# Optimization experiments

Measured on AMD Instinct MI355X. Metric: run time of the kernel, lower is better.

## Reference

```python
import jax, jax.numpy as jnp
import numpy as np
from jax import lax

DILATIONS = (1, 3, 9, 9, 3, 1)  # six mid blocks after the 1x1 input conv


def bilinear_sample(fm, verts):
    # fm: [B,H,W,C]; verts: [B,N,2] in [-1,1]; axis 0 of verts maps to H, axis 1 to W.
    # Matches jax.scipy.ndimage.map_coordinates(order=1, mode='constant'):
    # each out-of-bounds corner contributes 0.
    B, H, W, C = fm.shape
    scale = jnp.array([H - 1, W - 1], fm.dtype) / 2.0
    coords = (verts + 1.0) * scale  # [B,N,2]
    vy, vx = coords[..., 0], coords[..., 1]
    y0 = jnp.floor(vy)
    x0 = jnp.floor(vx)
    wy = (vy - y0)[..., None]
    wx = (vx - x0)[..., None]
    y0i = y0.astype(jnp.int32)
    x0i = x0.astype(jnp.int32)
    fm_flat = fm.reshape(B, H * W, C)

    def corner(yi, xi):
        valid = (yi >= 0) & (yi < H) & (xi >= 0) & (xi < W)
        idx = jnp.clip(yi, 0, H - 1) * W + jnp.clip(xi, 0, W - 1)  # [B,N]
        vals = jnp.take_along_axis(fm_flat, idx[..., None], axis=1)  # [B,N,C]
        return jnp.where(valid[..., None], vals, jnp.zeros((), fm.dtype))

    return ((1 - wy) * (1 - wx) * corner(y0i, x0i)
            + (1 - wy) * wx * corner(y0i, x0i + 1)
            + wy * (1 - wx) * corner(y0i + 1, x0i)
            + wy * wx * corner(y0i + 1, x0i + 1))


def conv1d(x, w, b, dil):
    # x: [B,N,Cin], w: [K,Cin,Cout]; flax nnx.Conv default: stride 1, SAME padding.
    out = lax.conv_general_dilated(x, w, (1,), 'SAME', rhs_dilation=(dil,),
                                   dimension_numbers=('NWC', 'WIO', 'NWC'))
    return out if b is None else out + b


def setup_inputs() -> dict:
    key = jax.random.key(0)
    ks = jax.random.split(key, 8)
    B, N, H, W, Cf, Ch = 16, 1024, 256, 256, 126, 512
    D = Cf + 2
    vertices = jax.random.uniform(ks[0], (B, N, 2), jnp.float32, -1.0, 1.0)
    feature_map = jax.random.normal(ks[1], (B, H, W, Cf), jnp.float32)
    w0 = jax.random.normal(ks[2], (1, D, Ch), jnp.float32) / np.float32(np.sqrt(D))
    b0 = jnp.zeros((Ch,), jnp.float32)
    ws = jax.random.normal(ks[3], (6, 3, Ch, Ch), jnp.float32) / np.float32(np.sqrt(3 * Ch))
    bs = jnp.zeros((6, Ch), jnp.float32)
    w_off = jax.random.normal(ks[4], (1, Ch, 2), jnp.float32) / np.float32(np.sqrt(Ch))
    return {"vertices": vertices, "feature_map": feature_map,
            "w0": w0, "b0": b0, "ws": ws, "bs": bs, "w_off": w_off}


def reference(vertices, feature_map, w0, b0, ws, bs, w_off):
    feat = bilinear_sample(feature_map, vertices)          # [B,N,Cf]
    x = jnp.concatenate([feat, vertices], axis=-1)         # [B,N,Cf+2]
    x = jax.nn.relu(conv1d(x, w0, b0, 1))                  # 1x1 input conv
    for i, dil in enumerate(DILATIONS):                    # fixed 6-layer stack
        x = jax.nn.relu(conv1d(x, ws[i], bs[i], dil))
    return conv1d(x, w_off, None, 1)                       # [B,N,2] offsets
```

## Files before the change

### kernel.cpp

```cpp
#include <hip/hip_runtime.h>

typedef __attribute__((ext_vector_type(4))) float f32x4;
typedef __attribute__((ext_vector_type(8))) _Float16 f16x8;

#define BM 128
#define BK 64

#define OFF_W0T 0
#define OFF_WT  131072
#define OFF_X0  (OFF_WT + 6*512*1536*2)
#define OFF_Y0  (OFF_X0 + 16384*128*2)
#define OFF_Y1  (OFF_Y0 + 16*1056*512*2)

__device__ __forceinline__ void load_lds16(const void* g, void* s) {
    __builtin_amdgcn_global_load_lds(
        (const __attribute__((address_space(1))) void*)g,
        (__attribute__((address_space(3))) void*)s, 16, 0, 0);
}

__global__ __launch_bounds__(256)
void wprep(const float* __restrict__ ws, const float* __restrict__ w0,
           _Float16* __restrict__ wt, _Float16* __restrict__ w0t)
{
    __shared__ float t[64][65];
    const int tid = threadIdx.x;
    const int tr = tid >> 6;
    const int tc = tid & 63;
    const int z = blockIdx.z;
    if (z < 18) {
        const int l = z / 3, tp = z % 3;
        const float* src = ws + (size_t)z * 512 * 512;
        const int ci0 = blockIdx.y * 64, co0 = blockIdx.x * 64;
        #pragma unroll
        for (int i = 0; i < 16; ++i) { int r = i*4 + tr; t[r][tc] = src[(ci0 + r)*512 + co0 + tc]; }
        __syncthreads();
        _Float16* dst = wt + (size_t)l * 512 * 1536;
        #pragma unroll
        for (int i = 0; i < 16; ++i) { int r = i*4 + tr; dst[(co0 + r)*1536 + tp*512 + ci0 + tc] = (_Float16)t[tc][r]; }
    } else {
        if (blockIdx.y >= 2) return;
        const int ci0 = blockIdx.y * 64, co0 = blockIdx.x * 64;
        #pragma unroll
        for (int i = 0; i < 16; ++i) { int r = i*4 + tr; t[r][tc] = w0[(ci0 + r)*512 + co0 + tc]; }
        __syncthreads();
        #pragma unroll
        for (int i = 0; i < 16; ++i) { int r = i*4 + tr; w0t[(co0 + r)*128 + ci0 + tc] = (_Float16)t[tc][r]; }
    }
}

__global__ __launch_bounds__(256)
void zeropad(_Float16* __restrict__ Y0, _Float16* __restrict__ Y1)
{
    const int i = blockIdx.x * 256 + threadIdx.x;
    const unsigned c2   = i & 255;
    const unsigned t2   = ((unsigned)i) >> 8;
    const unsigned prow = t2 & 31;
    const unsigned b    = (t2 >> 5) & 15;
    const unsigned buf  = t2 >> 9;
    const unsigned row  = prow < 16 ? prow : (1024 + prow);
    unsigned* p = (unsigned*)(buf ? Y1 : Y0);
    p[((size_t)b * 1056 + row) * 256 + c2] = 0u;
}

__global__ __launch_bounds__(256)
void sample_kernel(const float* __restrict__ verts, const float* __restrict__ fm,
                   _Float16* __restrict__ X0)
{
    const int p = blockIdx.x * 4 + (threadIdx.x >> 6);
    const int lane = threadIdx.x & 63;
    const int b = p >> 10;
    const float vy = verts[p*2], vx = verts[p*2 + 1];
    const float cy = (vy + 1.f) * 127.5f;
    const float cx = (vx + 1.f) * 127.5f;
    const float fy = floorf(cy), fx = floorf(cx);
    const int y0 = (int)fy, x0 = (int)fx;
    const float wy = cy - fy, wx = cx - fx;
    float w00 = (1.f - wy) * (1.f - wx), w01 = (1.f - wy) * wx;
    float w10 = wy * (1.f - wx),         w11 = wy * wx;
    const bool vy0 = (unsigned)y0 < 256u, vy1 = (unsigned)(y0 + 1) < 256u;
    const bool vx0 = (unsigned)x0 < 256u, vx1 = (unsigned)(x0 + 1) < 256u;
    w00 = (vy0 && vx0) ? w00 : 0.f;
    w01 = (vy0 && vx1) ? w01 : 0.f;
    w10 = (vy1 && vx0) ? w10 : 0.f;
    w11 = (vy1 && vx1) ? w11 : 0.f;
    const int yc0 = min(max(y0, 0), 255), yc1 = min(max(y0 + 1, 0), 255);
    const int xc0 = min(max(x0, 0), 255), xc1 = min(max(x0 + 1, 0), 255);
    const float* base = fm + (size_t)b * (256 * 256 * 126);
    const float* p00 = base + (yc0 * 256 + xc0) * 126;
    const float* p01 = base + (yc0 * 256 + xc1) * 126;
    const float* p10 = base + (yc1 * 256 + xc0) * 126;
    const float* p11 = base + (yc1 * 256 + xc1) * 126;
    _Float16* xr = X0 + (size_t)p * 128;
    for (int c = lane; c < 126; c += 64) {
        float a = w00 * p00[c] + w01 * p01[c] + w10 * p10[c] + w11 * p11[c];
        xr[c] = (_Float16)a;
    }
    if (lane < 2) xr[126 + lane] = (_Float16)(lane ? vx : vy);
}

template<int KTOT>
__global__ __launch_bounds__(256)
void conv_gemm(const _Float16* __restrict__ A, int a_row_stride, int a_batch_stride,
               const _Float16* __restrict__ WT, const float* __restrict__ bias,
               _Float16* __restrict__ Out, int o_row_stride, int o_batch_stride,
               int dil)
{
    __shared__ _Float16 Ald[BM * BK];
    __shared__ _Float16 Bld[BM * BK];
    const int tid  = threadIdx.x;
    const int wid  = tid >> 6;
    const int lane = tid & 63;
    const int b    = blockIdx.x >> 3;
    const int n0   = (blockIdx.x & 7) * BM;
    const int co0  = blockIdx.y * BM;
    const int wm   = wid >> 1, wn = wid & 1;

    const _Float16* Ab = A + (size_t)b * a_batch_stride + (size_t)n0 * a_row_stride;

    f32x4 acc[4][4] = {};

    const int srow = lane >> 3;
    const int scol = (lane & 7) * 8;

    for (int ks = 0; ks < KTOT / BK; ++ks) {
        int ci0, shift;
        if (KTOT == 128) { ci0 = ks * 64; shift = 0; }
        else             { int t = ks >> 3; ci0 = (ks & 7) * 64; shift = (t - 1) * dil; }
        const _Float16* Arow = Ab + (long)shift * a_row_stride + ci0 + scol;
        const _Float16* Brow = WT + (size_t)co0 * KTOT + ks * 64 + scol;
        #pragma unroll
        for (int i = 0; i < 4; ++i) {
            const int r0 = wid * 32 + i * 8;
            load_lds16(Arow + (size_t)(r0 + srow) * a_row_stride, &Ald[r0 * BK]);
            load_lds16(Brow + (size_t)(r0 + srow) * KTOT,         &Bld[r0 * BK]);
        }
        __syncthreads();
        #pragma unroll
        for (int kf = 0; kf < 2; ++kf) {
            f16x8 af[4], bfr[4];
            #pragma unroll
            for (int f = 0; f < 4; ++f) {
                af[f]  = *(const f16x8*)&Ald[(wm*64 + f*16 + (lane & 15)) * BK + kf*32 + (lane >> 4) * 8];
                bfr[f] = *(const f16x8*)&Bld[(wn*64 + f*16 + (lane & 15)) * BK + kf*32 + (lane >> 4) * 8];
            }
            #pragma unroll
            for (int m = 0; m < 4; ++m)
                #pragma unroll
                for (int n = 0; n < 4; ++n)
                    acc[m][n] = __builtin_amdgcn_mfma_f32_16x16x32_f16(af[m], bfr[n], acc[m][n], 0, 0, 0);
        }
        __syncthreads();
    }

    _Float16* Ob = Out + (size_t)b * o_batch_stride + (size_t)n0 * o_row_stride;
    #pragma unroll
    for (int n = 0; n < 4; ++n) {
        const int co = co0 + wn*64 + n*16 + (lane & 15);
        const float bv = bias[co];
        #pragma unroll
        for (int m = 0; m < 4; ++m) {
            #pragma unroll
            for (int j = 0; j < 4; ++j) {
                const int row = wm*64 + m*16 + (lane >> 4)*4 + j;
                float v = acc[m][n][j] + bv;
                v = fmaxf(v, 0.f);
                Ob[(size_t)row * o_row_stride + co] = (_Float16)v;
            }
        }
    }
}

#define NT8 24
__global__ __launch_bounds__(512, 2)
void conv_gemm8(const _Float16* __restrict__ A, const _Float16* __restrict__ WT,
                const float* __restrict__ bias, _Float16* __restrict__ Out, int dil)
{
    extern __shared__ _Float16 smem[];
    _Float16* Ald = smem;
    _Float16* Bld = smem + 3 * 256 * 64;

    const int tid  = threadIdx.x;
    const int wid  = tid >> 6;
    const int lane = tid & 63;
    const int wm   = wid >> 1;
    const int wn   = wid & 1;

    const int orig = blockIdx.x;
    const int swz  = (orig & 7) * 32 + (orig >> 3);
    const int nblk = swz & 3;
    const int mblk = swz >> 2;
    const int b     = mblk >> 2;
    const int n0row = (mblk & 3) * 256;
    const int co0   = nblk * 128;

    const _Float16* Ab = A + (size_t)b * (1056 * 512) + (size_t)n0row * 512;

    const int srow = lane >> 3;
    const int scol = (((lane & 7) ^ (lane >> 3)) << 3);

    f32x4 acc[4][4] = {};

    auto stageA = [&](int kt, int c, int ci0, int shift) {
        const int grow = 64 * c + 8 * wid + srow;
        const _Float16* src = Ab + (long)(grow + shift) * 512 + ci0 + scol;
        _Float16* dst = Ald + (kt % 3) * (256 * 64) + (64 * c + 8 * wid) * 64;
        load_lds16(src, dst);
    };
    auto stageB = [&](int kt, int c, int kk) {
        const int grow = 64 * c + 8 * wid + srow;
        const _Float16* src = WT + (size_t)(co0 + grow) * 1536 + kk + scol;
        _Float16* dst = Bld + (kt % 3) * (128 * 64) + (64 * c + 8 * wid) * 64;
        load_lds16(src, dst);
    };
    auto kinfo = [&](int ks, int& ci0, int& shift) {
        const int t = ks >> 3; ci0 = (ks & 7) * 64; shift = (t - 1) * dil;
    };

    {
        int ci0, sh;
        kinfo(0, ci0, sh);
        stageA(0, 0, ci0, sh); stageA(0, 1, ci0, sh); stageA(0, 2, ci0, sh); stageA(0, 3, ci0, sh);
        stageB(0, 0, 0); stageB(0, 1, 0);
        kinfo(1, ci0, sh);
        stageA(1, 0, ci0, sh); stageA(1, 1, ci0, sh); stageA(1, 2, ci0, sh); stageA(1, 3, ci0, sh);
        stageB(1, 0, 64); stageB(1, 1, 64);
    }

    for (int kt = 0; kt < NT8; ++kt) {
        __builtin_amdgcn_sched_barrier(0);
        if (kt < NT8 - 1) asm volatile("s_waitcnt vmcnt(6)" ::: "memory");
        else              asm volatile("s_waitcnt vmcnt(0)" ::: "memory");
        __builtin_amdgcn_s_barrier();
        __builtin_amdgcn_sched_barrier(0);

        const _Float16* Abuf = Ald + (kt % 3) * (256 * 64);
        const _Float16* Bbuf = Bld + (kt % 3) * (128 * 64);
        const bool do_stage = (kt + 2 < NT8);
        int nci0 = 0, nsh = 0;
        if (do_stage) kinfo(kt + 2, nci0, nsh);

        f16x8 bfr[4][2], af[4][2];
        #pragma unroll
        for (int nf = 0; nf < 4; ++nf) {
            const int row = wn * 64 + nf * 16 + (lane & 15);
            #pragma unroll
            for (int kf = 0; kf < 2; ++kf) {
                const int slot = (kf * 4 + (lane >> 4)) ^ (row & 7);
                bfr[nf][kf] = *(const f16x8*)&Bbuf[row * 64 + slot * 8];
            }
        }
        #pragma unroll
        for (int mf = 0; mf < 4; ++mf) {
            const int row = wm * 64 + mf * 16 + (lane & 15);
            #pragma unroll
            for (int kf = 0; kf < 2; ++kf) {
                const int slot = (kf * 4 + (lane >> 4)) ^ (row & 7);
                af[mf][kf] = *(const f16x8*)&Abuf[row * 64 + slot * 8];
            }
        }
        if (do_stage) {
            stageA(kt + 2, 0, nci0, nsh);
            stageA(kt + 2, 1, nci0, nsh);
            stageA(kt + 2, 2, nci0, nsh);
            stageA(kt + 2, 3, nci0, nsh);
            stageB(kt + 2, 0, (kt + 2) * 64);
            stageB(kt + 2, 1, (kt + 2) * 64);
        }
        __builtin_amdgcn_s_setprio(1);
        #pragma unroll
        for (int mf = 0; mf < 4; ++mf)
            #pragma unroll
            for (int nf = 0; nf < 4; ++nf)
                #pragma unroll
                for (int kf = 0; kf < 2; ++kf)
                    acc[mf][nf] = __builtin_amdgcn_mfma_f32_16x16x32_f16(
                        af[mf][kf], bfr[nf][kf], acc[mf][nf], 0, 0, 0);
        __builtin_amdgcn_s_setprio(0);
    }

    _Float16* Ob = Out + (size_t)b * (1056 * 512) + (size_t)n0row * 512;
    #pragma unroll
    for (int nf = 0; nf < 4; ++nf) {
        const int co = co0 + wn * 64 + nf * 16 + (lane & 15);
        const float bv = bias[co];
        #pragma unroll
        for (int m = 0; m < 4; ++m) {
            #pragma unroll
            for (int j = 0; j < 4; ++j) {
                const int row = wm * 64 + m * 16 + (lane >> 4) * 4 + j;
                float v = acc[m][nf][j] + bv;
                v = fmaxf(v, 0.f);
                Ob[(size_t)row * 512 + co] = (_Float16)v;
            }
        }
    }
}

__global__ __launch_bounds__(256)
void final_conv(const _Float16* __restrict__ Y, const float* __restrict__ woff,
                float* __restrict__ out)
{
    const int r = blockIdx.x * 4 + (threadIdx.x >> 6);
    const int lane = threadIdx.x & 63;
    const int b = r >> 10, n = r & 1023;
    const _Float16* yp = Y + ((size_t)b * 1056 + n) * 512 + lane * 8;
    f16x8 yv = *(const f16x8*)yp;
    const int ci0 = lane * 8;
    float s0 = 0.f, s1 = 0.f;
    #pragma unroll
    for (int e = 0; e < 8; ++e) {
        float y = (float)yv[e];
        s0 += y * woff[(ci0 + e) * 2 + 0];
        s1 += y * woff[(ci0 + e) * 2 + 1];
    }
    #pragma unroll
    for (int off = 32; off; off >>= 1) {
        s0 += __shfl_down(s0, off);
        s1 += __shfl_down(s1, off);
    }
    if (lane == 0) { out[r*2] = s0; out[r*2 + 1] = s1; }
}

extern "C" void kernel_launch(void* const* d_in, const int* in_sizes, int n_in,
                              void* d_out, int out_size, void* d_ws, size_t ws_size,
                              hipStream_t stream)
{
    const float* verts = (const float*)d_in[0];
    const float* fm    = (const float*)d_in[1];
    const float* w0    = (const float*)d_in[2];
    const float* b0    = (const float*)d_in[3];
    const float* ws    = (const float*)d_in[4];
    const float* bs    = (const float*)d_in[5];
    const float* woff  = (const float*)d_in[6];
    float* out = (float*)d_out;

    char* wsp = (char*)d_ws;
    _Float16* W0T = (_Float16*)(wsp + OFF_W0T);
    _Float16* WT  = (_Float16*)(wsp + OFF_WT);
    _Float16* X0  = (_Float16*)(wsp + OFF_X0);
    _Float16* Y0  = (_Float16*)(wsp + OFF_Y0);
    _Float16* Y1  = (_Float16*)(wsp + OFF_Y1);
    _Float16* Y0i = Y0 + 16 * 512;
    _Float16* Y1i = Y1 + 16 * 512;

    hipFuncSetAttribute(reinterpret_cast<const void*>(&conv_gemm8),
                        hipFuncAttributeMaxDynamicSharedMemorySize, 147456);

    wprep<<<dim3(8, 8, 19), 256, 0, stream>>>(ws, w0, WT, W0T);
    zeropad<<<1024, 256, 0, stream>>>(Y0, Y1);
    sample_kernel<<<4096, 256, 0, stream>>>(verts, fm, X0);

    conv_gemm<128><<<dim3(128, 4), 256, 0, stream>>>(
        X0, 128, 1024 * 128, W0T, b0, Y0i, 512, 1056 * 512, 1);

    const int DIL[6] = {1, 3, 9, 9, 3, 1};
    _Float16* bufs[2] = {Y0i, Y1i};
    for (int l = 0; l < 6; ++l) {
        conv_gemm8<<<256, 512, 147456, stream>>>(
            bufs[l & 1],
            WT + (size_t)l * 512 * 1536, bs + (size_t)l * 512,
            bufs[(l + 1) & 1], DIL[l]);
    }

    final_conv<<<4096, 256, 0, stream>>>(bufs[0], woff, out);
}
```

Before: 201.7 us.

## Load conv weight fragments directly from global memory instead of LDS staging

The dilated conv GEMM kernel no longer stages the weight (B) tiles through a triple-buffered LDS ring. Each wave now loads its B fragments straight from global memory into registers at the start of every k-step. LDS use drops to just the activation ring, and the dynamic shared memory request shrinks to match. The trade-off is that the weight loads are not prefetched, so their global or L2 latency is exposed every iteration. The four waves that share the same weight columns also each fetch them separately.

```diff
diff --git a/kernel.cpp b/kernel.cpp
--- a/kernel.cpp
+++ b/kernel.cpp
@@ -177,7 +177,6 @@
 {
     extern __shared__ _Float16 smem[];
     _Float16* Ald = smem;
-    _Float16* Bld = smem + 3 * 256 * 64;
 
     const int tid  = threadIdx.x;
     const int wid  = tid >> 6;
@@ -198,6 +197,8 @@
     const int srow = lane >> 3;
     const int scol = (((lane & 7) ^ (lane >> 3)) << 3);
 
+    const _Float16* WB = WT + (size_t)(co0 + wn * 64 + (lane & 15)) * 1536 + (lane >> 4) * 8;
+
     f32x4 acc[4][4] = {};
 
     auto stageA = [&](int kt, int c, int ci0, int shift) {
@@ -206,12 +207,6 @@
         _Float16* dst = Ald + (kt % 3) * (256 * 64) + (64 * c + 8 * wid) * 64;
         load_lds16(src, dst);
     };
-    auto stageB = [&](int kt, int c, int kk) {
-        const int grow = 64 * c + 8 * wid + srow;
-        const _Float16* src = WT + (size_t)(co0 + grow) * 1536 + kk + scol;
-        _Float16* dst = Bld + (kt % 3) * (128 * 64) + (64 * c + 8 * wid) * 64;
-        load_lds16(src, dst);
-    };
     auto kinfo = [&](int ks, int& ci0, int& shift) {
         const int t = ks >> 3; ci0 = (ks & 7) * 64; shift = (t - 1) * dil;
     };
@@ -220,35 +215,26 @@
         int ci0, sh;
         kinfo(0, ci0, sh);
         stageA(0, 0, ci0, sh); stageA(0, 1, ci0, sh); stageA(0, 2, ci0, sh); stageA(0, 3, ci0, sh);
-        stageB(0, 0, 0); stageB(0, 1, 0);
         kinfo(1, ci0, sh);
         stageA(1, 0, ci0, sh); stageA(1, 1, ci0, sh); stageA(1, 2, ci0, sh); stageA(1, 3, ci0, sh);
-        stageB(1, 0, 64); stageB(1, 1, 64);
     }
 
     for (int kt = 0; kt < NT8; ++kt) {
         __builtin_amdgcn_sched_barrier(0);
-        if (kt < NT8 - 1) asm volatile("s_waitcnt vmcnt(6)" ::: "memory");
-        else              asm volatile("s_waitcnt vmcnt(0)" ::: "memory");
+        asm volatile("s_waitcnt vmcnt(4)" ::: "memory");
         __builtin_amdgcn_s_barrier();
         __builtin_amdgcn_sched_barrier(0);
 
+        f16x8 bfr[4][2];
+        #pragma unroll
+        for (int nf = 0; nf < 4; ++nf)
+            #pragma unroll
+            for (int kf = 0; kf < 2; ++kf)
+                bfr[nf][kf] = *(const f16x8*)(WB + nf * 16 * 1536 + kt * 64 + kf * 32);
+        __builtin_amdgcn_sched_barrier(0);
+
         const _Float16* Abuf = Ald + (kt % 3) * (256 * 64);
-        const _Float16* Bbuf = Bld + (kt % 3) * (128 * 64);
-        const bool do_stage = (kt + 2 < NT8);
-        int nci0 = 0, nsh = 0;
-        if (do_stage) kinfo(kt + 2, nci0, nsh);
-
-        f16x8 bfr[4][2], af[4][2];
-        #pragma unroll
-        for (int nf = 0; nf < 4; ++nf) {
-            const int row = wn * 64 + nf * 16 + (lane & 15);
-            #pragma unroll
-            for (int kf = 0; kf < 2; ++kf) {
-                const int slot = (kf * 4 + (lane >> 4)) ^ (row & 7);
-                bfr[nf][kf] = *(const f16x8*)&Bbuf[row * 64 + slot * 8];
-            }
-        }
+        f16x8 af[4][2];
         #pragma unroll
         for (int mf = 0; mf < 4; ++mf) {
             const int row = wm * 64 + mf * 16 + (lane & 15);
@@ -258,14 +244,15 @@
                 af[mf][kf] = *(const f16x8*)&Abuf[row * 64 + slot * 8];
             }
         }
-        if (do_stage) {
+        if (kt + 2 < NT8) {
+            int nci0, nsh; kinfo(kt + 2, nci0, nsh);
             stageA(kt + 2, 0, nci0, nsh);
             stageA(kt + 2, 1, nci0, nsh);
             stageA(kt + 2, 2, nci0, nsh);
             stageA(kt + 2, 3, nci0, nsh);
-            stageB(kt + 2, 0, (kt + 2) * 64);
-            stageB(kt + 2, 1, (kt + 2) * 64);
-        }
+        }
+        __builtin_amdgcn_sched_barrier(0);
+
         __builtin_amdgcn_s_setprio(1);
         #pragma unroll
         for (int mf = 0; mf < 4; ++mf)
@@ -344,7 +331,7 @@
     _Float16* Y1i = Y1 + 16 * 512;
 
     hipFuncSetAttribute(reinterpret_cast<const void*>(&conv_gemm8),
-                        hipFuncAttributeMaxDynamicSharedMemorySize, 147456);
+                        hipFuncAttributeMaxDynamicSharedMemorySize, 98304);
 
     wprep<<<dim3(8, 8, 19), 256, 0, stream>>>(ws, w0, WT, W0T);
     zeropad<<<1024, 256, 0, stream>>>(Y0, Y1);
@@ -356,7 +343,7 @@
     const int DIL[6] = {1, 3, 9, 9, 3, 1};
     _Float16* bufs[2] = {Y0i, Y1i};
     for (int l = 0; l < 6; ++l) {
-        conv_gemm8<<<256, 512, 147456, stream>>>(
+        conv_gemm8<<<256, 512, 98304, stream>>>(
             bufs[l & 1],
             WT + (size_t)l * 512 * 1536, bs + (size_t)l * 512,
             bufs[(l + 1) & 1], DIL[l]);
```

Measured after the change: 441.8 us. +119.0%, slower.

## Split K across warp groups in conv_gemm8 and reduce partials through LDS

Applied to the files above, without the earlier changes.

The 8 warps are regrouped into two K-halves of four warps each. Every warp now covers a 128x64 output tile over half of each 64-wide K slice, so it does 8 A-fragment loads and 4 B-fragment loads per 32 MFMAs instead of 8 and 8. This cuts LDS read traffic per MFMA. In exchange, accumulator registers double to 32 f32x4 per warp and the epilogue adds an LDS reduction with extra barriers, which adds register pressure against the launch bound of two blocks per CU.

```diff
diff --git a/kernel.cpp b/kernel.cpp
--- a/kernel.cpp
+++ b/kernel.cpp
@@ -182,8 +182,10 @@
     const int tid  = threadIdx.x;
     const int wid  = tid >> 6;
     const int lane = tid & 63;
-    const int wm   = wid >> 1;
-    const int wn   = wid & 1;
+    const int q    = wid & 3;
+    const int sk   = wid >> 2;
+    const int wm   = q >> 1;
+    const int wn   = q & 1;
 
     const int orig = blockIdx.x;
     const int swz  = (orig & 7) * 32 + (orig >> 3);
@@ -198,7 +200,7 @@
     const int srow = lane >> 3;
     const int scol = (((lane & 7) ^ (lane >> 3)) << 3);
 
-    f32x4 acc[4][4] = {};
+    f32x4 acc[8][4] = {};
 
     auto stageA = [&](int kt, int c, int ci0, int shift) {
         const int grow = 64 * c + 8 * wid + srow;
@@ -239,24 +241,18 @@
         int nci0 = 0, nsh = 0;
         if (do_stage) kinfo(kt + 2, nci0, nsh);
 
-        f16x8 bfr[4][2], af[4][2];
+        f16x8 bfr[4], af[8];
         #pragma unroll
         for (int nf = 0; nf < 4; ++nf) {
             const int row = wn * 64 + nf * 16 + (lane & 15);
-            #pragma unroll
-            for (int kf = 0; kf < 2; ++kf) {
-                const int slot = (kf * 4 + (lane >> 4)) ^ (row & 7);
-                bfr[nf][kf] = *(const f16x8*)&Bbuf[row * 64 + slot * 8];
-            }
-        }
-        #pragma unroll
-        for (int mf = 0; mf < 4; ++mf) {
-            const int row = wm * 64 + mf * 16 + (lane & 15);
-            #pragma unroll
-            for (int kf = 0; kf < 2; ++kf) {
-                const int slot = (kf * 4 + (lane >> 4)) ^ (row & 7);
-                af[mf][kf] = *(const f16x8*)&Abuf[row * 64 + slot * 8];
-            }
+            const int slot = (sk * 4 + (lane >> 4)) ^ (row & 7);
+            bfr[nf] = *(const f16x8*)&Bbuf[row * 64 + slot * 8];
+        }
+        #pragma unroll
+        for (int mf = 0; mf < 8; ++mf) {
+            const int row = wm * 128 + mf * 16 + (lane & 15);
+            const int slot = (sk * 4 + (lane >> 4)) ^ (row & 7);
+            af[mf] = *(const f16x8*)&Abuf[row * 64 + slot * 8];
         }
         if (do_stage) {
             stageA(kt + 2, 0, nci0, nsh);
@@ -266,31 +262,49 @@
             stageB(kt + 2, 0, (kt + 2) * 64);
             stageB(kt + 2, 1, (kt + 2) * 64);
         }
+        __builtin_amdgcn_sched_barrier(0);
+
         __builtin_amdgcn_s_setprio(1);
         #pragma unroll
-        for (int mf = 0; mf < 4; ++mf)
+        for (int mf = 0; mf < 8; ++mf)
             #pragma unroll
             for (int nf = 0; nf < 4; ++nf)
-                #pragma unroll
-                for (int kf = 0; kf < 2; ++kf)
-                    acc[mf][nf] = __builtin_amdgcn_mfma_f32_16x16x32_f16(
-                        af[mf][kf], bfr[nf][kf], acc[mf][nf], 0, 0, 0);
+                acc[mf][nf] = __builtin_amdgcn_mfma_f32_16x16x32_f16(
+                    af[mf], bfr[nf], acc[mf][nf], 0, 0, 0);
         __builtin_amdgcn_s_setprio(0);
     }
 
+    float* red = (float*)smem;
     _Float16* Ob = Out + (size_t)b * (1056 * 512) + (size_t)n0row * 512;
     #pragma unroll
-    for (int nf = 0; nf < 4; ++nf) {
-        const int co = co0 + wn * 64 + nf * 16 + (lane & 15);
-        const float bv = bias[co];
-        #pragma unroll
-        for (int m = 0; m < 4; ++m) {
-            #pragma unroll
-            for (int j = 0; j < 4; ++j) {
-                const int row = wm * 64 + m * 16 + (lane >> 4) * 4 + j;
-                float v = acc[m][nf][j] + bv;
-                v = fmaxf(v, 0.f);
-                Ob[(size_t)row * 512 + co] = (_Float16)v;
+    for (int half = 0; half < 2; ++half) {
+        __builtin_amdgcn_s_barrier();
+        if (sk == 1) {
+            #pragma unroll
+            for (int mfl = 0; mfl < 4; ++mfl)
+                #pragma unroll
+                for (int nf = 0; nf < 4; ++nf)
+                    *(f32x4*)&red[(((q * 4 + mfl) * 4 + nf) * 64 + lane) * 4] =
+                        acc[half * 4 + mfl][nf];
+        }
+        __builtin_amdgcn_s_barrier();
+        if (sk == 0) {
+            #pragma unroll
+            for (int nf = 0; nf < 4; ++nf) {
+                const int co = co0 + wn * 64 + nf * 16 + (lane & 15);
+                const float bv = bias[co];
+                #pragma unroll
+                for (int mfl = 0; mfl < 4; ++mfl) {
+                    const int mf = half * 4 + mfl;
+                    f32x4 v = *(const f32x4*)&red[(((q * 4 + mfl) * 4 + nf) * 64 + lane) * 4];
+                    #pragma unroll
+                    for (int j = 0; j < 4; ++j) {
+                        const int row = wm * 128 + mf * 16 + (lane >> 4) * 4 + j;
+                        float val = acc[mf][nf][j] + v[j] + bv;
+                        val = fmaxf(val, 0.f);
+                        Ob[(size_t)row * 512 + co] = (_Float16)val;
+                    }
+                }
             }
         }
     }
```

Measured after the change: 202.3 us. No clear change (+0.3%).
